# Kernel tuning notes

Hardware: AMD Instinct MI355X
Metric: run time of the kernel (lower is better)

Reference implementation:

```python
import jax, jax.numpy as jnp
import numpy as np
from jax import lax

B, N, F_IN, DIM = 128, 200, 200, 32
E_PER = 6400
K1, K2 = 100, 50
OUT = 2
BN_EPS = 1e-5


def setup_inputs():
    key = jax.random.key(0)
    ks = jax.random.split(key, 16)
    x = jax.random.normal(ks[0], (B * N, F_IN), jnp.float32)
    src = jax.random.randint(ks[1], (B, E_PER), 0, N)
    dst = jax.random.randint(ks[2], (B, E_PER), 0, N)
    off = (jnp.arange(B) * N)[:, None]
    edge_index = jnp.stack([(src + off).reshape(-1), (dst + off).reshape(-1)]).astype(jnp.int32)
    batch = jnp.repeat(jnp.arange(B, dtype=jnp.int32), N)

    def lin(k, i, o):
        kw, kb = jax.random.split(k)
        return (jax.random.normal(kw, (i, o), jnp.float32) / np.float32(np.sqrt(i)),
                jax.random.normal(kb, (o,), jnp.float32) * 0.01)

    w1a, b1a = lin(ks[3], F_IN, DIM)
    w1b, b1b = lin(ks[4], DIM, DIM)
    w2a, b2a = lin(ks[5], DIM, DIM)
    w2b, b2b = lin(ks[6], DIM, DIM)
    pw1 = jax.random.normal(ks[7], (DIM,), jnp.float32)
    pw2 = jax.random.normal(ks[8], (DIM,), jnp.float32)
    fc1_w, fc1_b = lin(ks[9], 2 * DIM, 4 * DIM)
    fc2_w, fc2_b = lin(ks[10], 4 * DIM, 8 * DIM)
    fc3_w, fc3_b = lin(ks[11], 8 * DIM, OUT)
    return dict(x=x, edge_index=edge_index, batch=batch,
                w1a=w1a, b1a=b1a, w1b=w1b, b1b=b1b,
                w2a=w2a, b2a=b2a, w2b=w2b, b2b=b2b,
                pw1=pw1, pw2=pw2,
                fc1_w=fc1_w, fc1_b=fc1_b, fc2_w=fc2_w, fc2_b=fc2_b,
                fc3_w=fc3_w, fc3_b=fc3_b,
                bn1_g=jnp.ones((4 * DIM,)), bn1_b=jnp.zeros((4 * DIM,)),
                bn1_m=jnp.zeros((4 * DIM,)), bn1_v=jnp.ones((4 * DIM,)),
                bn2_g=jnp.ones((8 * DIM,)), bn2_b=jnp.zeros((8 * DIM,)),
                bn2_m=jnp.zeros((8 * DIM,)), bn2_v=jnp.ones((8 * DIM,)))


def gin_conv(x, src, dst, valid, wa, ba, wb, bb, n_nodes):
    # PyG GINConv: mlp((1+eps)*x + sum_{j->i} x_j), eps=0 (default)
    msg = x[src]
    if valid is not None:
        msg = msg * valid[:, None]
    aggr = jax.ops.segment_sum(msg, dst, num_segments=n_nodes)
    h = jax.nn.relu((x + aggr) @ wa + ba)
    return h @ wb + bb


def topk_pool(x, src, dst, valid, pw, nb, n_per, k):
    # PyG TopKPooling: score = tanh((x.w)/||w||); keep top-k per graph; x <- x[perm]*score[perm]
    score = jnp.tanh((x @ pw) / jnp.linalg.norm(pw))
    topv, topi = lax.top_k(score.reshape(nb, n_per), k)  # [nb,k], descending (matches PyG ordering)
    perm = (topi + (jnp.arange(nb) * n_per)[:, None]).reshape(-1)
    x_new = x[perm] * topv.reshape(-1, 1)
    new_id = jnp.full((nb * n_per,), -1, jnp.int32).at[perm].set(jnp.arange(nb * k, dtype=jnp.int32))
    s, d = new_id[src], new_id[dst]
    v = (s >= 0) & (d >= 0)
    if valid is not None:
        v = v & valid
    return x_new, jnp.maximum(s, 0), jnp.maximum(d, 0), v, topv


def bn_eval(h, g, b, m, v):
    return (h - m) * lax.rsqrt(v + BN_EPS) * g + b


def reference(x, edge_index, batch,
              w1a, b1a, w1b, b1b, w2a, b2a, w2b, b2b, pw1, pw2,
              fc1_w, fc1_b, fc2_w, fc2_b, fc3_w, fc3_b,
              bn1_g, bn1_b, bn1_m, bn1_v, bn2_g, bn2_b, bn2_m, bn2_v):
    src, dst = edge_index[0], edge_index[1]
    h = jax.nn.relu(gin_conv(x, src, dst, None, w1a, b1a, w1b, b1b, B * N))
    h, src, dst, valid, attn1 = topk_pool(h, src, dst, None, pw1, B, N, K1)
    hb = h.reshape(B, K1, DIM)
    x1 = jnp.concatenate([hb.max(axis=1), hb.mean(axis=1)], axis=1)  # gmp || gap
    h = jax.nn.relu(gin_conv(h, src, dst, valid.astype(h.dtype), w2a, b2a, w2b, b2b, B * K1))
    h, src, dst, valid, attn2 = topk_pool(h, src, dst, valid, pw2, B, K1, K2)
    hb = h.reshape(B, K2, DIM)
    x2 = jnp.concatenate([hb.max(axis=1), hb.mean(axis=1)], axis=1)
    z = x1 + x2
    z = bn_eval(jax.nn.relu(z @ fc1_w + fc1_b), bn1_g, bn1_b, bn1_m, bn1_v)  # dropout p=0.6 inactive (eval)
    z = bn_eval(jax.nn.relu(z @ fc2_w + fc2_b), bn2_g, bn2_b, bn2_m, bn2_v)
    xy = jax.nn.log_softmax(z @ fc3_w + fc3_b, axis=-1)
    return xy, jax.nn.sigmoid(attn1), jax.nn.sigmoid(attn2)
```

## Files before the change

### kernel.cpp

```cpp
#include <hip/hip_runtime.h>
#include <math.h>

#define NGRAPH 128
#define NNODE  200
#define FIN    200
#define DIM    32
#define EPER   6400
#define ETOT   819200
#define KP1    100
#define KP2    50

#define W1B_OFF  0
#define W2A_OFF  1024
#define W2B_OFF  2048
#define B1A_OFF  3072
#define B1B_OFF  3104
#define B2A_OFF  3136
#define B2B_OFF  3168
#define PW1_OFF  3200
#define PW2_OFF  3232
#define NRM1_OFF 3264
#define NRM2_OFF 3265
#define SW_SIZE  3280

__device__ __forceinline__ int swz(int row, int chunk) {
  return (row << 5) + (((chunk ^ ((row >> 2) & 7))) << 2);
}

__device__ __forceinline__ void spin_eq(const int* f, int target) {
  while (__hip_atomic_load(f, __ATOMIC_RELAXED,
                           __HIP_MEMORY_SCOPE_WORKGROUP) != target)
    __builtin_amdgcn_s_sleep(1);
}

template <int ROWS, bool RELU, bool BIAS, bool FUSE, bool SCORE>
__device__ __forceinline__ void mm2r(const float* __restrict__ A,
                                     const float* __restrict__ A2,
                                     const float* __restrict__ fb,
                                     const float* __restrict__ W,
                                     float* __restrict__ O,
                                     const float* __restrict__ bias,
                                     const float* __restrict__ pw,
                                     const float* __restrict__ nrmp,
                                     float* __restrict__ scoreOut, int tid) {
  if (tid < ROWS * 2) {
    const int rg = tid >> 2, cg = tid & 3;
    const int r0 = rg * 2, d0 = cg * 8;
    float acc[2][8];
#pragma unroll
    for (int r = 0; r < 2; ++r)
#pragma unroll
      for (int c = 0; c < 8; ++c) acc[r][c] = 0.f;
#pragma unroll
    for (int kc = 0; kc < 8; ++kc) {
      float4 av[2];
#pragma unroll
      for (int r = 0; r < 2; ++r) {
        const int p = swz(r0 + r, kc);
        float4 v = *(const float4*)&A[p];
        if (FUSE) {
          const float4 u = *(const float4*)&A2[p];
          const float4 b = *(const float4*)&fb[kc * 4];
          v.x = fmaxf(v.x + u.x + b.x, 0.f);
          v.y = fmaxf(v.y + u.y + b.y, 0.f);
          v.z = fmaxf(v.z + u.z + b.z, 0.f);
          v.w = fmaxf(v.w + u.w + b.w, 0.f);
        }
        av[r] = v;
      }
#pragma unroll
      for (int j = 0; j < 4; ++j) {
        const int k = kc * 4 + j;
        const float4 wa = *(const float4*)&W[k * 32 + d0];
        const float4 wb = *(const float4*)&W[k * 32 + d0 + 4];
#pragma unroll
        for (int r = 0; r < 2; ++r) {
          const float xs = (j == 0) ? av[r].x : (j == 1) ? av[r].y
                                  : (j == 2) ? av[r].z : av[r].w;
          acc[r][0] += xs * wa.x; acc[r][1] += xs * wa.y;
          acc[r][2] += xs * wa.z; acc[r][3] += xs * wa.w;
          acc[r][4] += xs * wb.x; acc[r][5] += xs * wb.y;
          acc[r][6] += xs * wb.z; acc[r][7] += xs * wb.w;
        }
      }
    }
    float dot[2] = {0.f, 0.f};
#pragma unroll
    for (int r = 0; r < 2; ++r) {
      float v[8];
#pragma unroll
      for (int c = 0; c < 8; ++c) {
        float t = acc[r][c];
        if (BIAS) t += bias[d0 + c];
        if (RELU) t = fmaxf(t, 0.f);
        v[c] = t;
      }
      if (SCORE) {
        float d = 0.f;
#pragma unroll
        for (int c = 0; c < 8; ++c) d += v[c] * pw[d0 + c];
        dot[r] = d;
      }
      float4 o0, o1;
      o0.x = v[0]; o0.y = v[1]; o0.z = v[2]; o0.w = v[3];
      o1.x = v[4]; o1.y = v[5]; o1.z = v[6]; o1.w = v[7];
      *(float4*)&O[swz(r0 + r, cg * 2)] = o0;
      *(float4*)&O[swz(r0 + r, cg * 2 + 1)] = o1;
    }
    if (SCORE) {
      dot[0] += __shfl_xor(dot[0], 1); dot[0] += __shfl_xor(dot[0], 2);
      dot[1] += __shfl_xor(dot[1], 1); dot[1] += __shfl_xor(dot[1], 2);
      if ((tid & 3) == 0) {
        const float nrm = *nrmp;
        scoreOut[r0] = tanhf(dot[0] / nrm);
        scoreOut[r0 + 1] = tanhf(dot[1] / nrm);
      }
    }
  }
}

__device__ __forceinline__ void scan_counts(const int* __restrict__ cnt,
                                            int* __restrict__ start, int lane) {
  const int b = lane * 4;
  const int c0 = (cnt[b + 0] + 3) & ~3;
  const int c1 = (cnt[b + 1] + 3) & ~3;
  const int c2 = (cnt[b + 2] + 3) & ~3;
  const int c3 = (cnt[b + 3] + 3) & ~3;
  const int t01 = c0 + c1;
  const int t012 = t01 + c2;
  const int tot = t012 + c3;
  int run = tot;
#pragma unroll
  for (int off = 1; off < 64; off <<= 1) {
    const int t = __shfl_up(run, off);
    if (lane >= off) run += t;
  }
  const int e = run - tot;
  start[b + 0] = e;
  start[b + 1] = e + c0;
  start[b + 2] = e + t01;
  start[b + 3] = e + t012;
}

template <int NN>
__device__ __forceinline__ void aggregate(const float* __restrict__ sYv,
                                          float* __restrict__ sAgv,
                                          const int* __restrict__ sSrcv,
                                          const int* __restrict__ sStartv,
                                          const int* __restrict__ sCntv, int tid) {
  const int slot = tid >> 3, part = tid & 7;
#pragma unroll
  for (int p = 0; p < (NN + 127) / 128; ++p) {
    const int n = p * 128 + slot;
    if (n < NN) {
      const int jb = sStartv[n];
      const int je = jb + sCntv[n];
      float4 a0 = {0, 0, 0, 0}, a1 = {0, 0, 0, 0}, a2 = {0, 0, 0, 0}, a3 = {0, 0, 0, 0};
      int j = jb;
      for (; j + 4 <= je; j += 4) {
        const int4 ss = *(const int4*)&sSrcv[j];
        const float4 v0 = *(const float4*)&sYv[swz(ss.x, part)];
        const float4 v1 = *(const float4*)&sYv[swz(ss.y, part)];
        const float4 v2 = *(const float4*)&sYv[swz(ss.z, part)];
        const float4 v3 = *(const float4*)&sYv[swz(ss.w, part)];
        a0.x += v0.x; a0.y += v0.y; a0.z += v0.z; a0.w += v0.w;
        a1.x += v1.x; a1.y += v1.y; a1.z += v1.z; a1.w += v1.w;
        a2.x += v2.x; a2.y += v2.y; a2.z += v2.z; a2.w += v2.w;
        a3.x += v3.x; a3.y += v3.y; a3.z += v3.z; a3.w += v3.w;
      }
      for (; j < je; ++j) {
        const float4 v = *(const float4*)&sYv[swz(sSrcv[j], part)];
        a0.x += v.x; a0.y += v.y; a0.z += v.z; a0.w += v.w;
      }
      float4 o;
      o.x = (a0.x + a1.x) + (a2.x + a3.x);
      o.y = (a0.y + a1.y) + (a2.y + a3.y);
      o.z = (a0.z + a1.z) + (a2.z + a3.z);
      o.w = (a0.w + a1.w) + (a2.w + a3.w);
      *(float4*)&sAgv[swz(n, part)] = o;
    }
  }
}

__global__ __launch_bounds__(1024, 1) void gin_fused(
    const float* __restrict__ x, const int* __restrict__ ei,
    const float* __restrict__ w1a, const float* __restrict__ b1a,
    const float* __restrict__ w1b, const float* __restrict__ b1b,
    const float* __restrict__ w2a, const float* __restrict__ b2a,
    const float* __restrict__ w2b, const float* __restrict__ b2b,
    const float* __restrict__ pw1, const float* __restrict__ pw2,
    const float* __restrict__ fc1w, const float* __restrict__ fc1b,
    const float* __restrict__ fc2w, const float* __restrict__ fc2b,
    const float* __restrict__ fc3w, const float* __restrict__ fc3b,
    const float* __restrict__ bn1g, const float* __restrict__ bn1b,
    const float* __restrict__ bn1m, const float* __restrict__ bn1v,
    const float* __restrict__ bn2g, const float* __restrict__ bn2b,
    const float* __restrict__ bn2m, const float* __restrict__ bn2v,
    float* __restrict__ out) {
  __shared__ __align__(16) float sY[6400];
  __shared__ __align__(16) float sAg[6400];
  __shared__ __align__(16) float sH[6400];
  __shared__ __align__(16) float sHp[3200];
  __shared__ __align__(16) float sW[SW_SIZE];
  __shared__ __align__(16) int sSrc[7040];
  __shared__ unsigned short sEdge[6400];
  __shared__ int sCnt[256], sStart[256], sOfs[256];
  __shared__ int sCnt2[256], sStart2[256], sOfs2[256];
  __shared__ int sFlag[8];
  __shared__ float sScore[256];
  __shared__ int sNewid[256];
  __shared__ float sZ[64];
  __shared__ float sZ1[128];

  const int tid = threadIdx.x;
  const int lane = tid & 63;
  const int g = blockIdx.x;

  if (tid < 8) sFlag[tid] = 0;
  __syncthreads();

  if (tid < 256) {
    for (int i = tid; i < 1600; i += 256)
      ((float4*)sAg)[i] = ((const float4*)w1a)[i];
    __threadfence_block();
    if (lane == 0) atomicAdd(&sFlag[0], 1);
    spin_eq(&sFlag[0], 4);
    if (tid < 200) {
      const int rg = tid >> 2, cg = tid & 3;
      const int n0 = rg * 4, d0 = cg * 8;
      float acc[4][8];
#pragma unroll
      for (int r = 0; r < 4; ++r)
#pragma unroll
        for (int c = 0; c < 8; ++c) acc[r][c] = 0.f;
      const float* xg = x + ((size_t)g * NNODE + n0) * FIN;
      for (int k = 0; k < FIN; k += 8) {
        float4 xv[4][2];
#pragma unroll
        for (int r = 0; r < 4; ++r) {
          xv[r][0] = *(const float4*)&xg[r * FIN + k];
          xv[r][1] = *(const float4*)&xg[r * FIN + k + 4];
        }
#pragma unroll
        for (int h = 0; h < 2; ++h) {
#pragma unroll
          for (int j = 0; j < 4; ++j) {
            const int kk = k + h * 4 + j;
            const float4 wa = *(const float4*)&sAg[kk * 32 + d0];
            const float4 wb = *(const float4*)&sAg[kk * 32 + d0 + 4];
#pragma unroll
            for (int r = 0; r < 4; ++r) {
              const float xs = (j == 0) ? xv[r][h].x : (j == 1) ? xv[r][h].y
                             : (j == 2) ? xv[r][h].z : xv[r][h].w;
              acc[r][0] += xs * wa.x; acc[r][1] += xs * wa.y;
              acc[r][2] += xs * wa.z; acc[r][3] += xs * wa.w;
              acc[r][4] += xs * wb.x; acc[r][5] += xs * wb.y;
              acc[r][6] += xs * wb.z; acc[r][7] += xs * wb.w;
            }
          }
        }
      }
#pragma unroll
      for (int r = 0; r < 4; ++r) {
        float4 o0, o1;
        o0.x = acc[r][0]; o0.y = acc[r][1]; o0.z = acc[r][2]; o0.w = acc[r][3];
        o1.x = acc[r][4]; o1.y = acc[r][5]; o1.z = acc[r][6]; o1.w = acc[r][7];
        *(float4*)&sY[swz(n0 + r, cg * 2)] = o0;
        *(float4*)&sY[swz(n0 + r, cg * 2 + 1)] = o1;
      }
    } else {
      const int t = tid - 200;
      if (t < 32) {
        sW[B1A_OFF + t] = b1a[t];
        sW[B1B_OFF + t] = b1b[t];
        sW[B2A_OFF + t] = b2a[t];
        sW[B2B_OFF + t] = b2b[t];
        sW[PW1_OFF + t] = pw1[t];
        sW[PW2_OFF + t] = pw2[t];
      }
      __threadfence_block();
      if (tid == 232) {
        float s = 0.f;
        for (int k = 0; k < 32; ++k) s += sW[PW1_OFF + k] * sW[PW1_OFF + k];
        sW[NRM1_OFF] = sqrtf(s);
      } else if (tid == 233) {
        float s = 0.f;
        for (int k = 0; k < 32; ++k) s += sW[PW2_OFF + k] * sW[PW2_OFF + k];
        sW[NRM2_OFF] = sqrtf(s);
      }
    }
  } else {
    const int t = tid - 256;
    if (t < 256) { sCnt[t] = 0; sOfs[t] = 0; sCnt2[t] = 0; sOfs2[t] = 0; }
    {
      const int eb = g * EPER, nb = g * NNODE;
      for (int i = t; i < EPER / 4; i += 768) {
        const int4 ss = *(const int4*)&ei[eb + i * 4];
        const int4 dd = *(const int4*)&ei[ETOT + eb + i * 4];
        sEdge[i * 4 + 0] = (unsigned short)(((ss.x - nb) << 8) | (dd.x - nb));
        sEdge[i * 4 + 1] = (unsigned short)(((ss.y - nb) << 8) | (dd.y - nb));
        sEdge[i * 4 + 2] = (unsigned short)(((ss.z - nb) << 8) | (dd.z - nb));
        sEdge[i * 4 + 3] = (unsigned short)(((ss.w - nb) << 8) | (dd.w - nb));
      }
    }
    __threadfence_block();
    if (lane == 0) atomicAdd(&sFlag[1], 1);
    spin_eq(&sFlag[1], 12);
    for (int i = t; i < 800; i += 768) {
      const uint4 u = *(const uint4*)&sEdge[i * 8];
      atomicAdd(&sCnt[u.x & 255], 1);
      atomicAdd(&sCnt[(u.x >> 16) & 255], 1);
      atomicAdd(&sCnt[u.y & 255], 1);
      atomicAdd(&sCnt[(u.y >> 16) & 255], 1);
      atomicAdd(&sCnt[u.z & 255], 1);
      atomicAdd(&sCnt[(u.z >> 16) & 255], 1);
      atomicAdd(&sCnt[u.w & 255], 1);
      atomicAdd(&sCnt[(u.w >> 16) & 255], 1);
    }
    __threadfence_block();
    if (lane == 0) atomicAdd(&sFlag[2], 1);
    if (tid >= 960) {
      spin_eq(&sFlag[2], 12);
      scan_counts(sCnt, sStart, tid - 960);
      __threadfence_block();
      if (tid == 960) atomicExch(&sFlag[3], 1);
    }
    spin_eq(&sFlag[3], 1);
    for (int e = t; e < EPER; e += 768) {
      const unsigned short p = sEdge[e];
      sSrc[sStart[p & 255] + atomicAdd(&sOfs[p & 255], 1)] = p >> 8;
    }
    if (tid >= 512) {
      for (int i = tid - 512; i < 768; i += 512) {
        const float4 v = (i < 256) ? ((const float4*)w1b)[i]
                      : (i < 512) ? ((const float4*)w2a)[i - 256]
                                  : ((const float4*)w2b)[i - 512];
        const int off = (i < 256) ? W1B_OFF + i * 4
                      : (i < 512) ? W2A_OFF + (i - 256) * 4
                                  : W2B_OFF + (i - 512) * 4;
        *(float4*)&sW[off] = v;
      }
    }
  }
  __syncthreads();

  aggregate<NNODE>(sY, sAg, sSrc, sStart, sCnt, tid);
  __syncthreads();

  mm2r<200, true, true, true, true>(sY, sAg, &sW[B1A_OFF], &sW[W1B_OFF], sH,
                                    &sW[B1B_OFF], &sW[PW1_OFF], &sW[NRM1_OFF],
                                    sScore, tid);
  __syncthreads();

  if (tid < NNODE * 4) {
    const int n = tid >> 2, q = tid & 3;
    const float s = sScore[n];
    int r = 0;
    for (int m = q * 50; m < q * 50 + 50; ++m) {
      const float sm = sScore[m];
      r += (sm > s) || (sm == s && m < n);
    }
    r += __shfl_xor(r, 1);
    r += __shfl_xor(r, 2);
    if (q == 0) {
      sNewid[n] = (r < KP1) ? r : -1;
      if (r < KP1) out[2 * NGRAPH + g * KP1 + r] = 1.f / (1.f + expf(-s));
    }
    if (r < KP1) {
#pragma unroll
      for (int c = 0; c < 2; ++c) {
        const int ch = q * 2 + c;
        float4 v = *(const float4*)&sH[swz(n, ch)];
        v.x *= s; v.y *= s; v.z *= s; v.w *= s;
        *(float4*)&sHp[swz(r, ch)] = v;
      }
    }
  }
  __syncthreads();

  mm2r<KP1, false, false, false, false>(sHp, nullptr, nullptr, &sW[W2A_OFF],
                                        sY, nullptr, nullptr, nullptr, nullptr,
                                        tid);
  if (tid >= 256 && tid < 320) {
    const int l = tid - 256;
    const int idx = l & 31, seg = l >> 5;
    const int ch = idx >> 2, w = idx & 3;
    float m = -INFINITY, s = 0.f;
    for (int r = seg * 50; r < seg * 50 + 50; ++r) {
      const float v = sHp[swz(r, ch) + w];
      m = fmaxf(m, v); s += v;
    }
    m = fmaxf(m, __shfl_xor(m, 32));
    s += __shfl_xor(s, 32);
    if (seg == 0) {
      sZ[idx] = m;
      sZ[32 + idx] = s / (float)KP1;
    }
  } else if (tid >= 512) {
    for (int e = tid - 512; e < EPER; e += 512) {
      const unsigned short p = sEdge[e];
      const int s1 = sNewid[p >> 8], d1 = sNewid[p & 255];
      if (s1 >= 0 && d1 >= 0) atomicAdd(&sCnt2[d1], 1);
    }
    __threadfence_block();
    if (lane == 0) atomicAdd(&sFlag[4], 1);
    if (tid >= 960) {
      spin_eq(&sFlag[4], 8);
      scan_counts(sCnt2, sStart2, tid - 960);
      __threadfence_block();
      if (tid == 960) atomicExch(&sFlag[5], 1);
    }
    spin_eq(&sFlag[5], 1);
    for (int e = tid - 512; e < EPER; e += 512) {
      const unsigned short p = sEdge[e];
      const int s1 = sNewid[p >> 8], d1 = sNewid[p & 255];
      if (s1 >= 0 && d1 >= 0)
        sSrc[sStart2[d1] + atomicAdd(&sOfs2[d1], 1)] = s1;
    }
  }
  __syncthreads();

  aggregate<KP1>(sY, sAg, sSrc, sStart2, sCnt2, tid);
  __syncthreads();

  mm2r<KP1, true, true, true, true>(sY, sAg, &sW[B2A_OFF], &sW[W2B_OFF], sH,
                                    &sW[B2B_OFF], &sW[PW2_OFF], &sW[NRM2_OFF],
                                    sScore, tid);
  __syncthreads();

  if (tid < KP1 * 4) {
    const int n = tid >> 2, q = tid & 3;
    const float s = sScore[n];
    int r = 0;
    for (int m = q * 25; m < q * 25 + 25; ++m) {
      const float sm = sScore[m];
      r += (sm > s) || (sm == s && m < n);
    }
    r += __shfl_xor(r, 1);
    r += __shfl_xor(r, 2);
    if (q == 0) {
      sNewid[n] = (r < KP2) ? r : -1;
      if (r < KP2)
        out[2 * NGRAPH + NGRAPH * KP1 + g * KP2 + r] = 1.f / (1.f + expf(-s));
    }
    if (r < KP2) {
#pragma unroll
      for (int c = 0; c < 2; ++c) {
        const int ch = q * 2 + c;
        float4 v = *(const float4*)&sH[swz(n, ch)];
        v.x *= s; v.y *= s; v.z *= s; v.w *= s;
        *(float4*)&sHp[swz(r, ch)] = v;
      }
    }
  }
  __syncthreads();

  if (tid < 64) {
    const int c = tid & 31, seg = tid >> 5;
    const int ch = c >> 2, w = c & 3;
    float m = -INFINITY, s = 0.f;
    for (int r = seg * 25; r < seg * 25 + 25; ++r) {
      const float v = sHp[swz(r, ch) + w];
      m = fmaxf(m, v); s += v;
    }
    m = fmaxf(m, __shfl_xor(m, 32));
    s += __shfl_xor(s, 32);
    if (seg == 0) {
      sZ[c] += m;
      sZ[32 + c] += s / (float)KP2;
    }
    __threadfence_block();

    const int l = tid;
    float a1 = fc1b[l], a2 = fc1b[l + 64];
    for (int k = 0; k < 64; ++k) {
      const float zk = sZ[k];
      a1 += zk * fc1w[k * 128 + l];
      a2 += zk * fc1w[k * 128 + l + 64];
    }
    a1 = fmaxf(a1, 0.f);
    a1 = (a1 - bn1m[l]) * rsqrtf(bn1v[l] + 1e-5f) * bn1g[l] + bn1b[l];
    a2 = fmaxf(a2, 0.f);
    a2 = (a2 - bn1m[l + 64]) * rsqrtf(bn1v[l + 64] + 1e-5f) * bn1g[l + 64] +
         bn1b[l + 64];
    sZ1[l] = a1;
    sZ1[l + 64] = a2;
    __threadfence_block();

    const int o4 = l * 4;
    float b0 = fc2b[o4], b1 = fc2b[o4 + 1], b2 = fc2b[o4 + 2], b3 = fc2b[o4 + 3];
    for (int k = 0; k < 128; ++k) {
      const float zk = sZ1[k];
      const float4 wv = *(const float4*)&fc2w[k * 256 + o4];
      b0 += zk * wv.x; b1 += zk * wv.y; b2 += zk * wv.z; b3 += zk * wv.w;
    }
    const float4 bm = *(const float4*)&bn2m[o4];
    const float4 bv = *(const float4*)&bn2v[o4];
    const float4 bg = *(const float4*)&bn2g[o4];
    const float4 bb = *(const float4*)&bn2b[o4];
    b0 = (fmaxf(b0, 0.f) - bm.x) * rsqrtf(bv.x + 1e-5f) * bg.x + bb.x;
    b1 = (fmaxf(b1, 0.f) - bm.y) * rsqrtf(bv.y + 1e-5f) * bg.y + bb.y;
    b2 = (fmaxf(b2, 0.f) - bm.z) * rsqrtf(bv.z + 1e-5f) * bg.z + bb.z;
    b3 = (fmaxf(b3, 0.f) - bm.w) * rsqrtf(bv.w + 1e-5f) * bg.w + bb.w;

    float a0s = b0 * fc3w[(o4 + 0) * 2 + 0] + b1 * fc3w[(o4 + 1) * 2 + 0] +
                b2 * fc3w[(o4 + 2) * 2 + 0] + b3 * fc3w[(o4 + 3) * 2 + 0];
    float a1s = b0 * fc3w[(o4 + 0) * 2 + 1] + b1 * fc3w[(o4 + 1) * 2 + 1] +
                b2 * fc3w[(o4 + 2) * 2 + 1] + b3 * fc3w[(o4 + 3) * 2 + 1];
#pragma unroll
    for (int off = 32; off; off >>= 1) {
      a0s += __shfl_xor(a0s, off);
      a1s += __shfl_xor(a1s, off);
    }
    if (tid == 0) {
      const float l0 = a0s + fc3b[0], l1 = a1s + fc3b[1];
      const float mx = fmaxf(l0, l1);
      const float lse = mx + logf(expf(l0 - mx) + expf(l1 - mx));
      out[g * 2 + 0] = l0 - lse;
      out[g * 2 + 1] = l1 - lse;
    }
  }
}

extern "C" void kernel_launch(void* const* d_in, const int* in_sizes, int n_in,
                              void* d_out, int out_size, void* d_ws,
                              size_t ws_size, hipStream_t stream) {
  (void)in_sizes; (void)n_in; (void)out_size; (void)d_ws; (void)ws_size;
  gin_fused<<<NGRAPH, 1024, 0, stream>>>(
      (const float*)d_in[0], (const int*)d_in[1],
      (const float*)d_in[3], (const float*)d_in[4],
      (const float*)d_in[5], (const float*)d_in[6],
      (const float*)d_in[7], (const float*)d_in[8],
      (const float*)d_in[9], (const float*)d_in[10],
      (const float*)d_in[11], (const float*)d_in[12],
      (const float*)d_in[13], (const float*)d_in[14],
      (const float*)d_in[15], (const float*)d_in[16],
      (const float*)d_in[17], (const float*)d_in[18],
      (const float*)d_in[19], (const float*)d_in[20],
      (const float*)d_in[21], (const float*)d_in[22],
      (const float*)d_in[23], (const float*)d_in[24],
      (const float*)d_in[25], (const float*)d_in[26],
      (float*)d_out);
}
```

Before: 50.01 us.

## Rebalance prologue: load all inputs first, then spread GEMM over 800 threads

The prologue is rebuilt in two phases. First every staging task (weights, biases, edge packing, counter resets) is split across all 1024 threads, followed by one barrier. Then the x@W1a product runs on 800 threads with 2x4 output tiles instead of 200 threads with 4x8 tiles, while 192 threads build the CSR edge lists alongside it. This removes the spin-wait stage in front of the GEMM and puts more threads on its FMA work. In exchange each x row is loaded by more threads and registers per thread shrink, and the CSR build now has fewer threads.

Result: faster. 46.12 us, median of 2 (-7.8%).

```diff
diff --git a/kernel.cpp b/kernel.cpp
--- a/kernel.cpp
+++ b/kernel.cpp
@@ -216,97 +216,90 @@
   const int lane = tid & 63;
   const int g = blockIdx.x;
 
-  if (tid < 8) sFlag[tid] = 0;
-  __syncthreads();
-
   if (tid < 256) {
-    for (int i = tid; i < 1600; i += 256)
+    sCnt[tid] = 0; sOfs[tid] = 0; sCnt2[tid] = 0; sOfs2[tid] = 0;
+    if (tid < 8) sFlag[tid] = 0;
+    if (tid < 32) {
+      sW[B1A_OFF + tid] = b1a[tid];
+      sW[B1B_OFF + tid] = b1b[tid];
+      sW[B2A_OFF + tid] = b2a[tid];
+      sW[B2B_OFF + tid] = b2b[tid];
+      sW[PW1_OFF + tid] = pw1[tid];
+      sW[PW2_OFF + tid] = pw2[tid];
+    }
+  } else if (tid < 512) {
+    for (int i = tid - 256; i < 1600; i += 256)
       ((float4*)sAg)[i] = ((const float4*)w1a)[i];
-    __threadfence_block();
-    if (lane == 0) atomicAdd(&sFlag[0], 1);
-    spin_eq(&sFlag[0], 4);
-    if (tid < 200) {
-      const int rg = tid >> 2, cg = tid & 3;
-      const int n0 = rg * 4, d0 = cg * 8;
-      float acc[4][8];
-#pragma unroll
-      for (int r = 0; r < 4; ++r)
-#pragma unroll
-        for (int c = 0; c < 8; ++c) acc[r][c] = 0.f;
-      const float* xg = x + ((size_t)g * NNODE + n0) * FIN;
-      for (int k = 0; k < FIN; k += 8) {
-        float4 xv[4][2];
-#pragma unroll
-        for (int r = 0; r < 4; ++r) {
-          xv[r][0] = *(const float4*)&xg[r * FIN + k];
-          xv[r][1] = *(const float4*)&xg[r * FIN + k + 4];
+  } else {
+    const int t = tid - 512;
+    const int eb = g * EPER, nb = g * NNODE;
+    for (int i = t; i < EPER / 4; i += 512) {
+      const int4 ss = *(const int4*)&ei[eb + i * 4];
+      const int4 dd = *(const int4*)&ei[ETOT + eb + i * 4];
+      sEdge[i * 4 + 0] = (unsigned short)(((ss.x - nb) << 8) | (dd.x - nb));
+      sEdge[i * 4 + 1] = (unsigned short)(((ss.y - nb) << 8) | (dd.y - nb));
+      sEdge[i * 4 + 2] = (unsigned short)(((ss.z - nb) << 8) | (dd.z - nb));
+      sEdge[i * 4 + 3] = (unsigned short)(((ss.w - nb) << 8) | (dd.w - nb));
+    }
+    for (int i = t; i < 768; i += 512) {
+      const float4 v = (i < 256) ? ((const float4*)w1b)[i]
+                    : (i < 512) ? ((const float4*)w2a)[i - 256]
+                                : ((const float4*)w2b)[i - 512];
+      const int off = (i < 256) ? W1B_OFF + i * 4
+                    : (i < 512) ? W2A_OFF + (i - 256) * 4
+                                : W2B_OFF + (i - 512) * 4;
+      *(float4*)&sW[off] = v;
+    }
+  }
+  __syncthreads();
+
+  if (tid < 800) {
+    const int rg = tid >> 3, cg = tid & 7;
+    const int n0 = rg * 2, d0 = cg * 4;
+    float a0[4] = {0, 0, 0, 0}, a1[4] = {0, 0, 0, 0};
+    const float* xg = x + ((size_t)g * NNODE + n0) * FIN;
+    for (int k = 0; k < FIN; k += 8) {
+      const float4 xa0 = *(const float4*)&xg[k];
+      const float4 xa1 = *(const float4*)&xg[k + 4];
+      const float4 xb0 = *(const float4*)&xg[FIN + k];
+      const float4 xb1 = *(const float4*)&xg[FIN + k + 4];
+#pragma unroll
+      for (int h = 0; h < 2; ++h) {
+#pragma unroll
+        for (int j = 0; j < 4; ++j) {
+          const int kk = k + h * 4 + j;
+          const float4 w = *(const float4*)&sAg[kk * 32 + d0];
+          const float s0 = (h == 0) ? ((j == 0) ? xa0.x : (j == 1) ? xa0.y
+                                      : (j == 2) ? xa0.z : xa0.w)
+                                    : ((j == 0) ? xa1.x : (j == 1) ? xa1.y
+                                      : (j == 2) ? xa1.z : xa1.w);
+          const float s1 = (h == 0) ? ((j == 0) ? xb0.x : (j == 1) ? xb0.y
+                                      : (j == 2) ? xb0.z : xb0.w)
+                                    : ((j == 0) ? xb1.x : (j == 1) ? xb1.y
+                                      : (j == 2) ? xb1.z : xb1.w);
+          a0[0] += s0 * w.x; a0[1] += s0 * w.y;
+          a0[2] += s0 * w.z; a0[3] += s0 * w.w;
+          a1[0] += s1 * w.x; a1[1] += s1 * w.y;
+          a1[2] += s1 * w.z; a1[3] += s1 * w.w;
         }
-#pragma unroll
-        for (int h = 0; h < 2; ++h) {
-#pragma unroll
-          for (int j = 0; j < 4; ++j) {
-            const int kk = k + h * 4 + j;
-            const float4 wa = *(const float4*)&sAg[kk * 32 + d0];
-            const float4 wb = *(const float4*)&sAg[kk * 32 + d0 + 4];
-#pragma unroll
-            for (int r = 0; r < 4; ++r) {
-              const float xs = (j == 0) ? xv[r][h].x : (j == 1) ? xv[r][h].y
-                             : (j == 2) ? xv[r][h].z : xv[r][h].w;
-              acc[r][0] += xs * wa.x; acc[r][1] += xs * wa.y;
-              acc[r][2] += xs * wa.z; acc[r][3] += xs * wa.w;
-              acc[r][4] += xs * wb.x; acc[r][5] += xs * wb.y;
-              acc[r][6] += xs * wb.z; acc[r][7] += xs * wb.w;
-            }
-          }
-        }
-      }
-#pragma unroll
-      for (int r = 0; r < 4; ++r) {
-        float4 o0, o1;
-        o0.x = acc[r][0]; o0.y = acc[r][1]; o0.z = acc[r][2]; o0.w = acc[r][3];
-        o1.x = acc[r][4]; o1.y = acc[r][5]; o1.z = acc[r][6]; o1.w = acc[r][7];
-        *(float4*)&sY[swz(n0 + r, cg * 2)] = o0;
-        *(float4*)&sY[swz(n0 + r, cg * 2 + 1)] = o1;
-      }
-    } else {
-      const int t = tid - 200;
-      if (t < 32) {
-        sW[B1A_OFF + t] = b1a[t];
-        sW[B1B_OFF + t] = b1b[t];
-        sW[B2A_OFF + t] = b2a[t];
-        sW[B2B_OFF + t] = b2b[t];
-        sW[PW1_OFF + t] = pw1[t];
-        sW[PW2_OFF + t] = pw2[t];
-      }
-      __threadfence_block();
-      if (tid == 232) {
-        float s = 0.f;
-        for (int k = 0; k < 32; ++k) s += sW[PW1_OFF + k] * sW[PW1_OFF + k];
-        sW[NRM1_OFF] = sqrtf(s);
-      } else if (tid == 233) {
-        float s = 0.f;
-        for (int k = 0; k < 32; ++k) s += sW[PW2_OFF + k] * sW[PW2_OFF + k];
-        sW[NRM2_OFF] = sqrtf(s);
-      }
-    }
-  } else {
-    const int t = tid - 256;
-    if (t < 256) { sCnt[t] = 0; sOfs[t] = 0; sCnt2[t] = 0; sOfs2[t] = 0; }
-    {
-      const int eb = g * EPER, nb = g * NNODE;
-      for (int i = t; i < EPER / 4; i += 768) {
-        const int4 ss = *(const int4*)&ei[eb + i * 4];
-        const int4 dd = *(const int4*)&ei[ETOT + eb + i * 4];
-        sEdge[i * 4 + 0] = (unsigned short)(((ss.x - nb) << 8) | (dd.x - nb));
-        sEdge[i * 4 + 1] = (unsigned short)(((ss.y - nb) << 8) | (dd.y - nb));
-        sEdge[i * 4 + 2] = (unsigned short)(((ss.z - nb) << 8) | (dd.z - nb));
-        sEdge[i * 4 + 3] = (unsigned short)(((ss.w - nb) << 8) | (dd.w - nb));
-      }
-    }
-    __threadfence_block();
-    if (lane == 0) atomicAdd(&sFlag[1], 1);
-    spin_eq(&sFlag[1], 12);
-    for (int i = t; i < 800; i += 768) {
+      }
+    }
+    float4 o;
+    o.x = a0[0]; o.y = a0[1]; o.z = a0[2]; o.w = a0[3];
+    *(float4*)&sY[swz(n0, cg)] = o;
+    o.x = a1[0]; o.y = a1[1]; o.z = a1[2]; o.w = a1[3];
+    *(float4*)&sY[swz(n0 + 1, cg)] = o;
+  } else if (tid == 800) {
+    float s = 0.f;
+    for (int k = 0; k < 32; ++k) s += sW[PW1_OFF + k] * sW[PW1_OFF + k];
+    sW[NRM1_OFF] = sqrtf(s);
+  } else if (tid == 801) {
+    float s = 0.f;
+    for (int k = 0; k < 32; ++k) s += sW[PW2_OFF + k] * sW[PW2_OFF + k];
+    sW[NRM2_OFF] = sqrtf(s);
+  } else if (tid >= 832) {
+    const int t = tid - 832;
+    for (int i = t; i < 800; i += 192) {
       const uint4 u = *(const uint4*)&sEdge[i * 8];
       atomicAdd(&sCnt[u.x & 255], 1);
       atomicAdd(&sCnt[(u.x >> 16) & 255], 1);
@@ -318,28 +311,17 @@
       atomicAdd(&sCnt[(u.w >> 16) & 255], 1);
     }
     __threadfence_block();
-    if (lane == 0) atomicAdd(&sFlag[2], 1);
+    if (lane == 0) atomicAdd(&sFlag[1], 1);
     if (tid >= 960) {
-      spin_eq(&sFlag[2], 12);
+      spin_eq(&sFlag[1], 3);
       scan_counts(sCnt, sStart, tid - 960);
       __threadfence_block();
-      if (tid == 960) atomicExch(&sFlag[3], 1);
-    }
-    spin_eq(&sFlag[3], 1);
-    for (int e = t; e < EPER; e += 768) {
+      if (tid == 960) atomicExch(&sFlag[2], 1);
+    }
+    spin_eq(&sFlag[2], 1);
+    for (int e = t; e < EPER; e += 192) {
       const unsigned short p = sEdge[e];
       sSrc[sStart[p & 255] + atomicAdd(&sOfs[p & 255], 1)] = p >> 8;
-    }
-    if (tid >= 512) {
-      for (int i = tid - 512; i < 768; i += 512) {
-        const float4 v = (i < 256) ? ((const float4*)w1b)[i]
-                      : (i < 512) ? ((const float4*)w2a)[i - 256]
-                                  : ((const float4*)w2b)[i - 512];
-        const int off = (i < 256) ? W1B_OFF + i * 4
-                      : (i < 512) ? W2A_OFF + (i - 256) * 4
-                                  : W2B_OFF + (i - 512) * 4;
-        *(float4*)&sW[off] = v;
-      }
     }
   }
   __syncthreads();
```
